# Kernel tuning notes

Hardware: AMD Instinct MI355X
Metric: run time of the kernel (lower is better)

## Reference

```python
import jax, jax.numpy as jnp
import numpy as np

EPS = 1e-12  # torch F.normalize eps


def _l2norm(v, axis):
    return v / jnp.maximum(jnp.linalg.norm(v, axis=axis, keepdims=True), EPS)


def setup_inputs() -> dict:
    key = jax.random.key(0)
    k1, k2, k3 = jax.random.split(key, 3)
    N, D, H, W, K = 32, 512, 64, 64, 64
    x = jax.random.normal(k1, (N, D, H, W), dtype=jnp.float32)
    conv_w = jax.random.normal(k2, (K, D), dtype=jnp.float32) * 0.05
    centroids = jax.random.normal(k3, (K, D), dtype=jnp.float32)
    return {"x": x, "conv_w": conv_w, "centroids": centroids}


def reference(x, conv_w, centroids):
    # x: [N, D, H, W]; conv_w: [K, D] (1x1 conv, no bias); centroids: [K, D]
    N, D, H, W = x.shape
    K = conv_w.shape[0]
    # descriptor-wise L2 normalization over channel dim
    x = _l2norm(x, axis=1)
    xf = x.reshape(N, D, H * W)                      # [N, D, P]
    # 1x1 conv == matmul over channels; softmax over clusters
    logits = jnp.einsum('kd,ndp->nkp', conv_w, xf)    # [N, K, P]
    a = jax.nn.softmax(logits, axis=1)                # [N, K, P]
    # vlad[n,k,d] = sum_p a[n,k,p] * (xf[n,d,p] - c[k,d])
    #            = (a @ xf^T)[n,k,d] - (sum_p a[n,k,p]) * c[k,d]
    vlad = jnp.einsum('nkp,ndp->nkd', a, xf) \
         - a.sum(axis=-1)[:, :, None] * centroids[None, :, :]  # [N, K, D]
    vlad = _l2norm(vlad, axis=2)                      # intra-normalization
    v = vlad.reshape(N, K * D)
    return _l2norm(v, axis=1)                         # global L2 norm
```

## Files before the change

### kernel.cpp

```cpp
#include <hip/hip_runtime.h>
#include <hip/hip_bf16.h>
#include <math.h>

#define Nn 32
#define Dd 512
#define Pp 4096
#define Kk 64
#define PSEG 4
static constexpr float EPSF = 1e-12f;

typedef short short8 __attribute__((ext_vector_type(8)));
typedef float floatx4 __attribute__((ext_vector_type(4)));

static __device__ __forceinline__ int f2b2(float a, float b) {
  __hip_bfloat162 h = __float22bfloat162_rn(float2{a, b});
  int r; __builtin_memcpy(&r, &h, 4); return r;
}
static __device__ __forceinline__ short8 pack8(const float* v) {
  union { short8 s; int i[4]; } u;
  u.i[0] = f2b2(v[0], v[1]); u.i[1] = f2b2(v[2], v[3]);
  u.i[2] = f2b2(v[4], v[5]); u.i[3] = f2b2(v[6], v[7]);
  return u.s;
}
static __device__ __forceinline__ short f2b1(float f) {
  unsigned u = __float_as_uint(f);
  return (short)((u + 0x7FFFu + ((u >> 16) & 1u)) >> 16);
}
static __device__ __forceinline__ float b2f(short s) {
  return __uint_as_float(((unsigned)(unsigned short)s) << 16);
}

__global__ __launch_bounds__(256) void k_wpack(
    const float* __restrict__ w, short* __restrict__ wp)
{
  int id = blockIdx.x * 256 + threadIdx.x;
  int chunk = id >> 6, k = id & 63;
  const float* src = w + (size_t)k * Dd + chunk * 32;
  short* dst = wp + ((size_t)(chunk * 64 + k)) * 32;
#pragma unroll
  for (int q = 0; q < 4; ++q) {
    float v[8];
    *(float4*)&v[0] = *(const float4*)(src + q * 8);
    *(float4*)&v[4] = *(const float4*)(src + q * 8 + 4);
    *(short8*)(dst + q * 8) = pack8(v);
  }
}

__global__ __launch_bounds__(256) void k_assign(
    const float* __restrict__ x, const short* __restrict__ wp,
    short* __restrict__ a_s, float* __restrict__ asum)
{
  __shared__ short ab4[4][2048];
  __shared__ float invs[128];

  const int tid = threadIdx.x;
  const int n  = blockIdx.x >> 5;
  const int p0 = (blockIdx.x & 31) * 128;
  const int wave = tid >> 6, lane = tid & 63;
  const int q = lane >> 4, pc = lane & 15;
  const int wpx = wave * 32;

  floatx4 acc[4][2];
#pragma unroll
  for (int t = 0; t < 4; ++t)
#pragma unroll
    for (int s = 0; s < 2; ++s) acc[t][s] = floatx4{0.f, 0.f, 0.f, 0.f};
  float sq[2] = {0.f, 0.f};

  const float* xa0 = x + (size_t)n * Dd * Pp + (size_t)(q * 8) * Pp + p0 + wpx + pc;
  const float* xa1 = xa0 + 16;

  for (int dc = 0; dc < Dd; dc += 32) {
    short8 bf[4];
    const short* wc = wp + (size_t)(dc >> 5) * 2048 + pc * 32 + q * 8;
#pragma unroll
    for (int t = 0; t < 4; ++t)
      bf[t] = *(const short8*)(wc + t * 512);
    float v0[8], v1[8];
#pragma unroll
    for (int j = 0; j < 8; ++j) {
      float a0 = xa0[(size_t)j * Pp];
      float a1 = xa1[(size_t)j * Pp];
      v0[j] = a0; v1[j] = a1;
      sq[0] += a0 * a0; sq[1] += a1 * a1;
    }
    short8 af0 = pack8(v0), af1 = pack8(v1);
#pragma unroll
    for (int t = 0; t < 4; ++t) {
      acc[t][0] = __builtin_amdgcn_mfma_f32_16x16x32_bf16(af0, bf[t], acc[t][0], 0, 0, 0);
      acc[t][1] = __builtin_amdgcn_mfma_f32_16x16x32_bf16(af1, bf[t], acc[t][1], 0, 0, 0);
    }
    xa0 += (size_t)32 * Pp; xa1 += (size_t)32 * Pp;
  }

#pragma unroll
  for (int s = 0; s < 2; ++s) {
    float t = sq[s];
    t += __shfl_xor(t, 16);
    t += __shfl_xor(t, 32);
    if (q == 0) invs[wpx + s * 16 + pc] = 1.f / fmaxf(sqrtf(t), EPSF);
  }
  float ivr[2][4];
#pragma unroll
  for (int s = 0; s < 2; ++s)
#pragma unroll
    for (int r = 0; r < 4; ++r)
      ivr[s][r] = invs[wpx + s * 16 + q * 4 + r];

#pragma unroll
  for (int s = 0; s < 2; ++s)
#pragma unroll
    for (int r = 0; r < 4; ++r) {
      float l[4];
#pragma unroll
      for (int t = 0; t < 4; ++t) l[t] = acc[t][s][r] * ivr[s][r];
      float mx = fmaxf(fmaxf(l[0], l[1]), fmaxf(l[2], l[3]));
      mx = fmaxf(mx, __shfl_xor(mx, 1));
      mx = fmaxf(mx, __shfl_xor(mx, 2));
      mx = fmaxf(mx, __shfl_xor(mx, 4));
      mx = fmaxf(mx, __shfl_xor(mx, 8));
      float e[4], sm = 0.f;
#pragma unroll
      for (int t = 0; t < 4; ++t) { e[t] = __expf(l[t] - mx); sm += e[t]; }
      sm += __shfl_xor(sm, 1);
      sm += __shfl_xor(sm, 2);
      sm += __shfl_xor(sm, 4);
      sm += __shfl_xor(sm, 8);
      float si = 1.f / sm;
      int pl = s * 16 + q * 4 + r;
#pragma unroll
      for (int t = 0; t < 4; ++t)
        ab4[wave][(t * 16 + pc) * 32 + pl] = f2b1(e[t] * si);
    }

#pragma unroll
  for (int pass = 0; pass < 4; ++pass) {
    int kr = pass * 16 + (lane >> 2);
    int c8 = (lane & 3) * 8;
    short8 av = *(short8*)&ab4[wave][kr * 32 + c8];
    float aw[8]; float s8 = 0.f;
#pragma unroll
    for (int i = 0; i < 8; ++i) { aw[i] = b2f(av[i]); s8 += aw[i]; }
    s8 += __shfl_down(s8, 1);
    s8 += __shfl_down(s8, 2);
    if ((lane & 3) == 0) atomicAdd(&asum[n * Kk + kr], s8);
    float ivv[8];
    *(float4*)&ivv[0] = *(const float4*)&invs[wpx + c8];
    *(float4*)&ivv[4] = *(const float4*)&invs[wpx + c8 + 4];
    float ov[8];
#pragma unroll
    for (int i = 0; i < 8; ++i) ov[i] = aw[i] * ivv[i];
    *(short8*)(a_s + ((size_t)(n * Kk + kr)) * Pp + p0 + wpx + c8) = pack8(ov);
  }
}

__global__ __launch_bounds__(256) void k_vlad(
    const float* __restrict__ x, const short* __restrict__ a_s,
    float* __restrict__ vpart)
{
  const int tid = threadIdx.x;
  const int ps = blockIdx.x & 3;
  const int dt = (blockIdx.x >> 2) & 3;
  const int n  = blockIdx.x >> 4;
  const int wave = tid >> 6, lane = tid & 63;
  const int q = lane >> 4, pc = lane & 15;
  const int dw = dt * 128 + wave * 32;
  const int pb = ps * (Pp / PSEG);

  floatx4 acc[4][2];
#pragma unroll
  for (int t = 0; t < 4; ++t)
#pragma unroll
    for (int s = 0; s < 2; ++s) acc[t][s] = floatx4{0.f, 0.f, 0.f, 0.f};

  const short* ab0 = a_s + ((size_t)(n * Kk + pc)) * Pp + q * 8;
  const float* xb0 = x + ((size_t)(n * Dd + dw + pc)) * Pp + q * 8;

#pragma unroll 2
  for (int p = pb; p < pb + Pp / PSEG; p += 32) {
    short8 af[4];
#pragma unroll
    for (int t = 0; t < 4; ++t)
      af[t] = *(const short8*)(ab0 + (size_t)t * 16 * Pp + p);
    short8 bf[2];
#pragma unroll
    for (int s = 0; s < 2; ++s) {
      const float* xp = xb0 + (size_t)s * 16 * Pp + p;
      float bv[8];
      *(float4*)&bv[0] = *(const float4*)xp;
      *(float4*)&bv[4] = *(const float4*)(xp + 4);
      bf[s] = pack8(bv);
    }
#pragma unroll
    for (int t = 0; t < 4; ++t)
#pragma unroll
      for (int s = 0; s < 2; ++s)
        acc[t][s] = __builtin_amdgcn_mfma_f32_16x16x32_bf16(af[t], bf[s], acc[t][s], 0, 0, 0);
  }

  float* vb = vpart + (((size_t)ps * Nn + n) * Kk) * Dd;
#pragma unroll
  for (int t = 0; t < 4; ++t)
#pragma unroll
    for (int s = 0; s < 2; ++s)
#pragma unroll
      for (int r = 0; r < 4; ++r)
        vb[(size_t)(t * 16 + q * 4 + r) * Dd + dw + s * 16 + pc] = acc[t][s][r];
}

__global__ __launch_bounds__(128) void k_intra(
    const float* __restrict__ vpart, const float* __restrict__ asum,
    const float* __restrict__ cent, float* __restrict__ out, float* __restrict__ gnsq)
{
  __shared__ float red[2];
  const int nk = blockIdx.x;
  const int n = nk >> 6, k = nk & 63;
  const int tid = threadIdx.x;
  const int d = tid * 4;

  float4 v = {0.f, 0.f, 0.f, 0.f};
#pragma unroll
  for (int ps = 0; ps < PSEG; ++ps) {
    float4 t = *(const float4*)&vpart[(((size_t)ps * Nn + n) * Kk + k) * Dd + d];
    v.x += t.x; v.y += t.y; v.z += t.z; v.w += t.w;
  }
  float s = asum[n * Kk + k];
  float4 c = *(const float4*)&cent[(size_t)k * Dd + d];
  v.x -= s * c.x; v.y -= s * c.y; v.z -= s * c.z; v.w -= s * c.w;

  float qq = v.x * v.x + v.y * v.y + v.z * v.z + v.w * v.w;
#pragma unroll
  for (int off = 32; off; off >>= 1) qq += __shfl_down(qq, off);
  if ((tid & 63) == 0) red[tid >> 6] = qq;
  __syncthreads();
  float norm = sqrtf(red[0] + red[1]);
  float r = 1.f / fmaxf(norm, EPSF);
  v.x *= r; v.y *= r; v.z *= r; v.w *= r;
  *(float4*)&out[(size_t)n * (Kk * Dd) + (size_t)k * Dd + d] = v;
  if (tid == 0) {
    float t = norm * r;
    atomicAdd(&gnsq[n], t * t);
  }
}

__global__ __launch_bounds__(256) void k_gscale(
    float* __restrict__ out, const float* __restrict__ gnsq)
{
  size_t i = ((size_t)blockIdx.x * 256 + threadIdx.x) * 4;
  int n = (int)(i >> 15);
  float r = 1.f / fmaxf(sqrtf(gnsq[n]), EPSF);
  float4 v = *(float4*)&out[i];
  v.x *= r; v.y *= r; v.z *= r; v.w *= r;
  *(float4*)&out[i] = v;
}

extern "C" void kernel_launch(void* const* d_in, const int* in_sizes, int n_in,
                              void* d_out, int out_size, void* d_ws, size_t ws_size,
                              hipStream_t stream) {
  (void)in_sizes; (void)n_in; (void)out_size; (void)ws_size;
  const float* x    = (const float*)d_in[0];
  const float* w    = (const float*)d_in[1];
  const float* cent = (const float*)d_in[2];
  float* out = (float*)d_out;

  short* a_s   = (short*)d_ws;
  float* asum  = (float*)(a_s + (size_t)Nn * Kk * Pp);
  float* gnsq  = asum + Nn * Kk;
  float* vpart = gnsq + 64;
  short* wpk   = (short*)(vpart + (size_t)PSEG * Nn * Kk * Dd);

  hipMemsetAsync(asum, 0, (Nn * Kk + 64) * sizeof(float), stream);
  k_wpack<<<4, 256, 0, stream>>>(w, wpk);
  k_assign<<<Nn * 32, 256, 0, stream>>>(x, wpk, a_s, asum);
  k_vlad<<<Nn * 4 * PSEG, 256, 0, stream>>>(x, a_s, vpart);
  k_intra<<<Nn * Kk, 128, 0, stream>>>(vpart, asum, cent, out, gnsq);
  k_gscale<<<(Nn * Kk * Dd) / (256 * 4), 256, 0, stream>>>(out, gnsq);
}
```

Baseline: 464.7 us.

## Fuse soft-assignment and VLAD aggregation into one kernel with LDS-staged x tiles

Merges the assignment kernel and the VLAD accumulation kernel into a single kernel. Each block handles a 256-pixel segment of one image in 64-pixel tiles, staging x as bf16 in shared memory, computing the softmax assignments into shared memory, then running the a·x^T MFMA from LDS. This removes the global round-trip of the assignment matrix and the second full read of x. Partial VLAD sums are now stored as bf16 across 16 segments, which adds rounding error and more partials for the intra-norm kernel to reduce; the large LDS footprint and accumulator count also limit occupancy.

```diff
diff --git a/kernel.cpp b/kernel.cpp
--- a/kernel.cpp
+++ b/kernel.cpp
@@ -6,10 +6,13 @@
 #define Dd 512
 #define Pp 4096
 #define Kk 64
-#define PSEG 4
+#define SEG 16
+#define PXB 256
+#define PT 64
 static constexpr float EPSF = 1e-12f;
 
 typedef short short8 __attribute__((ext_vector_type(8)));
+typedef short short4v __attribute__((ext_vector_type(4)));
 typedef float floatx4 __attribute__((ext_vector_type(4)));
 
 static __device__ __forceinline__ int f2b2(float a, float b) {
@@ -46,74 +49,82 @@
   }
 }
 
-__global__ __launch_bounds__(256) void k_assign(
+__global__ __launch_bounds__(256, 2) void k_fused(
     const float* __restrict__ x, const short* __restrict__ wp,
-    short* __restrict__ a_s, float* __restrict__ asum)
-{
-  __shared__ short ab4[4][2048];
-  __shared__ float invs[128];
+    float* __restrict__ asum, short* __restrict__ vpart)
+{
+  constexpr int XS = 64;
+  constexpr int AS = 72;
+  __shared__ short xb[Dd * XS];
+  __shared__ short as_[Kk * AS];
+  __shared__ float invs[PT];
 
   const int tid = threadIdx.x;
-  const int n  = blockIdx.x >> 5;
-  const int p0 = (blockIdx.x & 31) * 128;
+  const int n = blockIdx.x >> 4, seg = blockIdx.x & 15;
   const int wave = tid >> 6, lane = tid & 63;
   const int q = lane >> 4, pc = lane & 15;
-  const int wpx = wave * 32;
-
-  floatx4 acc[4][2];
+  const int sd = tid >> 3, sc = tid & 7;
+
+  floatx4 acc2[4][8];
 #pragma unroll
   for (int t = 0; t < 4; ++t)
 #pragma unroll
-    for (int s = 0; s < 2; ++s) acc[t][s] = floatx4{0.f, 0.f, 0.f, 0.f};
-  float sq[2] = {0.f, 0.f};
-
-  const float* xa0 = x + (size_t)n * Dd * Pp + (size_t)(q * 8) * Pp + p0 + wpx + pc;
-  const float* xa1 = xa0 + 16;
-
-  for (int dc = 0; dc < Dd; dc += 32) {
-    short8 bf[4];
-    const short* wc = wp + (size_t)(dc >> 5) * 2048 + pc * 32 + q * 8;
-#pragma unroll
-    for (int t = 0; t < 4; ++t)
-      bf[t] = *(const short8*)(wc + t * 512);
-    float v0[8], v1[8];
-#pragma unroll
-    for (int j = 0; j < 8; ++j) {
-      float a0 = xa0[(size_t)j * Pp];
-      float a1 = xa1[(size_t)j * Pp];
-      v0[j] = a0; v1[j] = a1;
-      sq[0] += a0 * a0; sq[1] += a1 * a1;
-    }
-    short8 af0 = pack8(v0), af1 = pack8(v1);
-#pragma unroll
-    for (int t = 0; t < 4; ++t) {
-      acc[t][0] = __builtin_amdgcn_mfma_f32_16x16x32_bf16(af0, bf[t], acc[t][0], 0, 0, 0);
-      acc[t][1] = __builtin_amdgcn_mfma_f32_16x16x32_bf16(af1, bf[t], acc[t][1], 0, 0, 0);
-    }
-    xa0 += (size_t)32 * Pp; xa1 += (size_t)32 * Pp;
-  }
-
-#pragma unroll
-  for (int s = 0; s < 2; ++s) {
-    float t = sq[s];
-    t += __shfl_xor(t, 16);
-    t += __shfl_xor(t, 32);
-    if (q == 0) invs[wpx + s * 16 + pc] = 1.f / fmaxf(sqrtf(t), EPSF);
-  }
-  float ivr[2][4];
-#pragma unroll
-  for (int s = 0; s < 2; ++s)
-#pragma unroll
-    for (int r = 0; r < 4; ++r)
-      ivr[s][r] = invs[wpx + s * 16 + q * 4 + r];
-
-#pragma unroll
-  for (int s = 0; s < 2; ++s)
+    for (int s2 = 0; s2 < 8; ++s2) acc2[t][s2] = floatx4{0.f, 0.f, 0.f, 0.f};
+  float asr[4] = {0.f, 0.f, 0.f, 0.f};
+
+  const float* xn = x + (size_t)n * Dd * Pp;
+
+  for (int pt = 0; pt < PXB / PT; ++pt) {
+    const int p0 = seg * PXB + pt * PT;
+    __syncthreads();
+
+    floatx4 acc1[4];
+#pragma unroll
+    for (int t = 0; t < 4; ++t) acc1[t] = floatx4{0.f, 0.f, 0.f, 0.f};
+    float sq = 0.f;
+
+    const float* xa = xn + (size_t)(q * 8) * Pp + p0 + wave * 16 + pc;
+    const float* xs = xn + (size_t)sd * Pp + p0 + sc * 8;
+
+    for (int dc = 0; dc < Dd; dc += 32) {
+      float4 u0 = *(const float4*)xs;
+      float4 u1 = *(const float4*)(xs + 4);
+      int2 w0 = { f2b2(u0.x, u0.y), f2b2(u0.z, u0.w) };
+      int2 w1 = { f2b2(u1.x, u1.y), f2b2(u1.z, u1.w) };
+      *(int2*)&xb[(dc + sd) * XS + sc * 8] = w0;
+      *(int2*)&xb[(dc + sd) * XS + sc * 8 + 4] = w1;
+      xs += (size_t)32 * Pp;
+      float v[8];
+#pragma unroll
+      for (int j = 0; j < 8; ++j) {
+        float a = xa[(size_t)j * Pp];
+        v[j] = a; sq += a * a;
+      }
+      xa += (size_t)32 * Pp;
+      short8 af = pack8(v);
+      const short* wc = wp + (size_t)(dc >> 5) * 2048 + pc * 32 + q * 8;
+#pragma unroll
+      for (int t = 0; t < 4; ++t) {
+        short8 bf = *(const short8*)(wc + t * 512);
+        acc1[t] = __builtin_amdgcn_mfma_f32_16x16x32_bf16(af, bf, acc1[t], 0, 0, 0);
+      }
+    }
+
+    {
+      float tsum = sq;
+      tsum += __shfl_xor(tsum, 16);
+      tsum += __shfl_xor(tsum, 32);
+      if (q == 0) invs[wave * 16 + pc] = 1.f / fmaxf(sqrtf(tsum), EPSF);
+    }
+    float ivr[4];
+#pragma unroll
+    for (int r = 0; r < 4; ++r) ivr[r] = invs[wave * 16 + q * 4 + r];
+
 #pragma unroll
     for (int r = 0; r < 4; ++r) {
       float l[4];
 #pragma unroll
-      for (int t = 0; t < 4; ++t) l[t] = acc[t][s][r] * ivr[s][r];
+      for (int t = 0; t < 4; ++t) l[t] = acc1[t][r] * ivr[r];
       float mx = fmaxf(fmaxf(l[0], l[1]), fmaxf(l[2], l[3]));
       mx = fmaxf(mx, __shfl_xor(mx, 1));
       mx = fmaxf(mx, __shfl_xor(mx, 2));
@@ -127,89 +138,51 @@
       sm += __shfl_xor(sm, 4);
       sm += __shfl_xor(sm, 8);
       float si = 1.f / sm;
-      int pl = s * 16 + q * 4 + r;
+#pragma unroll
+      for (int t = 0; t < 4; ++t) {
+        float av = e[t] * si;
+        asr[t] += av;
+        as_[(t * 16 + pc) * AS + wave * 16 + q * 4 + r] = f2b1(av * ivr[r]);
+      }
+    }
+    __syncthreads();
+
+#pragma unroll
+    for (int c = 0; c < 2; ++c) {
+      short8 af2[4];
 #pragma unroll
       for (int t = 0; t < 4; ++t)
-        ab4[wave][(t * 16 + pc) * 32 + pl] = f2b1(e[t] * si);
-    }
-
-#pragma unroll
-  for (int pass = 0; pass < 4; ++pass) {
-    int kr = pass * 16 + (lane >> 2);
-    int c8 = (lane & 3) * 8;
-    short8 av = *(short8*)&ab4[wave][kr * 32 + c8];
-    float aw[8]; float s8 = 0.f;
-#pragma unroll
-    for (int i = 0; i < 8; ++i) { aw[i] = b2f(av[i]); s8 += aw[i]; }
-    s8 += __shfl_down(s8, 1);
-    s8 += __shfl_down(s8, 2);
-    if ((lane & 3) == 0) atomicAdd(&asum[n * Kk + kr], s8);
-    float ivv[8];
-    *(float4*)&ivv[0] = *(const float4*)&invs[wpx + c8];
-    *(float4*)&ivv[4] = *(const float4*)&invs[wpx + c8 + 4];
-    float ov[8];
-#pragma unroll
-    for (int i = 0; i < 8; ++i) ov[i] = aw[i] * ivv[i];
-    *(short8*)(a_s + ((size_t)(n * Kk + kr)) * Pp + p0 + wpx + c8) = pack8(ov);
-  }
-}
-
-__global__ __launch_bounds__(256) void k_vlad(
-    const float* __restrict__ x, const short* __restrict__ a_s,
-    float* __restrict__ vpart)
-{
-  const int tid = threadIdx.x;
-  const int ps = blockIdx.x & 3;
-  const int dt = (blockIdx.x >> 2) & 3;
-  const int n  = blockIdx.x >> 4;
-  const int wave = tid >> 6, lane = tid & 63;
-  const int q = lane >> 4, pc = lane & 15;
-  const int dw = dt * 128 + wave * 32;
-  const int pb = ps * (Pp / PSEG);
-
-  floatx4 acc[4][2];
+        af2[t] = *(const short8*)&as_[(t * 16 + pc) * AS + c * 32 + q * 8];
+#pragma unroll
+      for (int s2 = 0; s2 < 8; ++s2) {
+        short8 bf2 = *(const short8*)&xb[(wave * 128 + s2 * 16 + pc) * XS + c * 32 + q * 8];
+#pragma unroll
+        for (int t = 0; t < 4; ++t)
+          acc2[t][s2] = __builtin_amdgcn_mfma_f32_16x16x32_bf16(af2[t], bf2, acc2[t][s2], 0, 0, 0);
+      }
+    }
+  }
+
+#pragma unroll
+  for (int t = 0; t < 4; ++t) {
+    float v = asr[t];
+    v += __shfl_xor(v, 16);
+    v += __shfl_xor(v, 32);
+    if (q == 0) atomicAdd(&asum[n * Kk + t * 16 + pc], v);
+  }
+  short* vb = vpart + ((size_t)(seg * Nn + n) * Kk) * Dd;
 #pragma unroll
   for (int t = 0; t < 4; ++t)
 #pragma unroll
-    for (int s = 0; s < 2; ++s) acc[t][s] = floatx4{0.f, 0.f, 0.f, 0.f};
-
-  const short* ab0 = a_s + ((size_t)(n * Kk + pc)) * Pp + q * 8;
-  const float* xb0 = x + ((size_t)(n * Dd + dw + pc)) * Pp + q * 8;
-
-#pragma unroll 2
-  for (int p = pb; p < pb + Pp / PSEG; p += 32) {
-    short8 af[4];
-#pragma unroll
-    for (int t = 0; t < 4; ++t)
-      af[t] = *(const short8*)(ab0 + (size_t)t * 16 * Pp + p);
-    short8 bf[2];
-#pragma unroll
-    for (int s = 0; s < 2; ++s) {
-      const float* xp = xb0 + (size_t)s * 16 * Pp + p;
-      float bv[8];
-      *(float4*)&bv[0] = *(const float4*)xp;
-      *(float4*)&bv[4] = *(const float4*)(xp + 4);
-      bf[s] = pack8(bv);
-    }
-#pragma unroll
-    for (int t = 0; t < 4; ++t)
-#pragma unroll
-      for (int s = 0; s < 2; ++s)
-        acc[t][s] = __builtin_amdgcn_mfma_f32_16x16x32_bf16(af[t], bf[s], acc[t][s], 0, 0, 0);
-  }
-
-  float* vb = vpart + (((size_t)ps * Nn + n) * Kk) * Dd;
-#pragma unroll
-  for (int t = 0; t < 4; ++t)
-#pragma unroll
-    for (int s = 0; s < 2; ++s)
+    for (int s2 = 0; s2 < 8; ++s2)
 #pragma unroll
       for (int r = 0; r < 4; ++r)
-        vb[(size_t)(t * 16 + q * 4 + r) * Dd + dw + s * 16 + pc] = acc[t][s][r];
+        vb[(size_t)(t * 16 + q * 4 + r) * Dd + wave * 128 + s2 * 16 + pc] =
+            f2b1(acc2[t][s2][r]);
 }
 
 __global__ __launch_bounds__(128) void k_intra(
-    const float* __restrict__ vpart, const float* __restrict__ asum,
+    const short* __restrict__ vpart, const float* __restrict__ asum,
     const float* __restrict__ cent, float* __restrict__ out, float* __restrict__ gnsq)
 {
   __shared__ float red[2];
@@ -220,9 +193,9 @@
 
   float4 v = {0.f, 0.f, 0.f, 0.f};
 #pragma unroll
-  for (int ps = 0; ps < PSEG; ++ps) {
-    float4 t = *(const float4*)&vpart[(((size_t)ps * Nn + n) * Kk + k) * Dd + d];
-    v.x += t.x; v.y += t.y; v.z += t.z; v.w += t.w;
+  for (int ps = 0; ps < SEG; ++ps) {
+    short4v t = *(const short4v*)&vpart[((size_t)(ps * Nn + n) * Kk + k) * Dd + d];
+    v.x += b2f(t[0]); v.y += b2f(t[1]); v.z += b2f(t[2]); v.w += b2f(t[3]);
   }
   float s = asum[n * Kk + k];
   float4 c = *(const float4*)&cent[(size_t)k * Dd + d];
@@ -263,16 +236,14 @@
   const float* cent = (const float*)d_in[2];
   float* out = (float*)d_out;
 
-  short* a_s   = (short*)d_ws;
-  float* asum  = (float*)(a_s + (size_t)Nn * Kk * Pp);
+  float* asum  = (float*)d_ws;
   float* gnsq  = asum + Nn * Kk;
-  float* vpart = gnsq + 64;
-  short* wpk   = (short*)(vpart + (size_t)PSEG * Nn * Kk * Dd);
+  short* vpart = (short*)(gnsq + 64);
+  short* wpk   = vpart + (size_t)SEG * Nn * Kk * Dd;
 
   hipMemsetAsync(asum, 0, (Nn * Kk + 64) * sizeof(float), stream);
   k_wpack<<<4, 256, 0, stream>>>(w, wpk);
-  k_assign<<<Nn * 32, 256, 0, stream>>>(x, wpk, a_s, asum);
-  k_vlad<<<Nn * 4 * PSEG, 256, 0, stream>>>(x, a_s, vpart);
+  k_fused<<<Nn * SEG, 256, 0, stream>>>(x, wpk, asum, vpart);
   k_intra<<<Nn * Kk, 128, 0, stream>>>(vpart, asum, cent, out, gnsq);
   k_gscale<<<(Nn * Kk * Dd) / (256 * 4), 256, 0, stream>>>(out, gnsq);
 }
```

Result: faster. 419.0 us (-9.8%).
